# Kernel optimization log

Measured on AMD Instinct MI355X. Metric: run time of the kernel, lower is better.

Reference implementation:

```python
import jax, jax.numpy as jnp
import numpy as np

N_SEND = 49152   # 12 * 64^2 HEALPix nodes
N_REC = 65536    # 256x256 receiver grid
N_EDGES = 262144 # N_REC * 4 nearest senders
D_MODEL = 256
EDGE_IN, EDGE_OUT = 4, 64
LIN_IN, LIN_OUT = 320, 256
B = 2


def setup_inputs() -> dict:
    key = jax.random.key(0)
    ks = jax.random.split(key, 8)
    x = jax.random.normal(ks[0], (B, N_SEND, D_MODEL), dtype=jnp.float32)
    senders = jax.random.randint(ks[1], (N_EDGES,), 0, N_SEND, dtype=jnp.int32)
    receivers = jax.random.randint(ks[2], (N_EDGES,), 0, N_REC, dtype=jnp.int32)
    edge_index = jnp.stack([senders, receivers], axis=0)
    edge_attr = jax.random.normal(ks[3], (N_EDGES, EDGE_IN), dtype=jnp.float32)
    s = lambda fan_in: 1.0 / np.sqrt(fan_in)
    return {
        "x": x,
        "edge_index": edge_index,
        "edge_attr": edge_attr,
        "ee_w1": jax.random.normal(ks[4], (EDGE_IN, EDGE_OUT), dtype=jnp.float32) * s(EDGE_IN),
        "ee_b1": jnp.zeros((EDGE_OUT,), dtype=jnp.float32),
        "ee_w2": jax.random.normal(ks[5], (EDGE_OUT, EDGE_OUT), dtype=jnp.float32) * s(EDGE_OUT),
        "ee_b2": jnp.zeros((EDGE_OUT,), dtype=jnp.float32),
        "ff_w1": jax.random.normal(ks[6], (LIN_IN, LIN_OUT), dtype=jnp.float32) * s(LIN_IN),
        "ff_b1": jnp.zeros((LIN_OUT,), dtype=jnp.float32),
        "ff_w2": jax.random.normal(ks[7], (LIN_OUT, LIN_OUT), dtype=jnp.float32) * s(LIN_OUT),
        "ff_b2": jnp.zeros((LIN_OUT,), dtype=jnp.float32),
    }


def reference(x, edge_index, edge_attr,
              ee_w1, ee_b1, ee_w2, ee_b2,
              ff_w1, ff_b1, ff_w2, ff_b2):
    senders, receivers = edge_index[0], edge_index[1]
    # edge embedder MLP: [E, edge_in] -> [E, edge_out]
    h = jax.nn.relu(edge_attr @ ee_w1 + ee_b1)
    edge_feat = h @ ee_w2 + ee_b2                       # [E, edge_out]
    # gather sender node features: [B, E, d_model]
    v_s = x[:, senders, :]
    # concat with broadcast edge features: [B, E, d_model + edge_out]
    ef = jnp.broadcast_to(edge_feat[None], (x.shape[0],) + edge_feat.shape)
    v_s_prime = jnp.concatenate([v_s, ef], axis=-1)
    # scatter-sum onto receiver nodes: [B, n_rec, lin_in]
    v_m_sum = jnp.zeros((x.shape[0], N_REC, v_s_prime.shape[-1]), dtype=x.dtype)
    v_m_sum = v_m_sum.at[:, receivers, :].add(v_s_prime)
    # g2m feedforward: [B, n_rec, lin_out]
    h2 = jax.nn.relu(v_m_sum @ ff_w1 + ff_b1)
    return h2 @ ff_w2 + ff_b2
```

## Files before the change

kernel.cpp:

```cpp
#include <hip/hip_runtime.h>
#include <hip/hip_bf16.h>

#define N_SEND 49152
#define N_REC  65536
#define N_EDGES 262144
#define D_MODEL 256
#define EDGE_IN 4
#define EDGE_OUT 64
#define LIN_IN 320
#define LIN_OUT 256
#define BATCH 2

#define GBM 64

typedef __attribute__((ext_vector_type(4))) float f32x4;
typedef __attribute__((ext_vector_type(8))) short bf16x8;

static __device__ __forceinline__ unsigned short f2bf(float f) {
    union { float f; unsigned u; } v; v.f = f;
    unsigned r = v.u + 0x7FFF + ((v.u >> 16) & 1);
    return (unsigned short)(r >> 16);
}
static __device__ __forceinline__ float bf2f(unsigned short h) {
    union { unsigned u; float f; } v; v.u = ((unsigned)h) << 16; return v.f;
}

static __device__ __forceinline__ void async_copy16(void* lds_ptr, const void* g_ptr) {
    __builtin_amdgcn_global_load_lds(
        (const __attribute__((address_space(1))) void*)g_ptr,
        (__attribute__((address_space(3))) void*)lds_ptr, 16, 0, 0);
}

__global__ __launch_bounds__(256) void prep_fused(
    const float* __restrict__ x, unsigned short* __restrict__ xb, int nconv,
    const int* __restrict__ receivers, const float* __restrict__ edge_attr,
    const float* __restrict__ ee_w1, const float* __restrict__ ee_b1,
    const float* __restrict__ ee_w2, const float* __restrict__ ee_b2,
    unsigned short* __restrict__ efs, int* __restrict__ counts,
    const float* __restrict__ w1, const float* __restrict__ w2,
    unsigned short* __restrict__ w1t, unsigned short* __restrict__ w2t)
{
    __shared__ __align__(16) unsigned short h_lds[256 * EDGE_OUT];

    const int bid = blockIdx.x;
    const int tid = threadIdx.x;

    if (bid < nconv) {
        const size_t i = ((size_t)bid * 256 + tid) * 8;
        const float4 v0 = *(const float4*)&x[i];
        const float4 v1 = *(const float4*)&x[i + 4];
        bf16x8 o;
        o[0] = (short)f2bf(v0.x); o[1] = (short)f2bf(v0.y);
        o[2] = (short)f2bf(v0.z); o[3] = (short)f2bf(v0.w);
        o[4] = (short)f2bf(v1.x); o[5] = (short)f2bf(v1.y);
        o[6] = (short)f2bf(v1.z); o[7] = (short)f2bf(v1.w);
        *(bf16x8*)&xb[i] = o;
        return;
    }
    const int b2 = bid - nconv;

    if (b2 < N_EDGES / 256) {
        const int e0 = b2 * 256;
        atomicAdd(&counts[receivers[e0 + tid]], 1);

        {
            const float4 ea = *(const float4*)&edge_attr[(size_t)(e0 + tid) * EDGE_IN];
#pragma unroll
            for (int kb = 0; kb < 8; ++kb) {
                bf16x8 hv;
#pragma unroll
                for (int j = 0; j < 8; ++j) {
                    const int k = kb * 8 + j;
                    float a = ee_b1[k];
                    a += ea.x * ee_w1[0 * EDGE_OUT + k];
                    a += ea.y * ee_w1[1 * EDGE_OUT + k];
                    a += ea.z * ee_w1[2 * EDGE_OUT + k];
                    a += ea.w * ee_w1[3 * EDGE_OUT + k];
                    hv[j] = (short)f2bf(fmaxf(a, 0.0f));
                }
                *(bf16x8*)&h_lds[tid * EDGE_OUT + ((kb ^ (tid & 7)) * 8)] = hv;
            }
        }

        const int lane = tid & 63, wave = tid >> 6;
        const int n16 = lane & 15, hi = lane >> 4;

        bf16x8 bfr[2][4];
#pragma unroll
        for (int ch = 0; ch < 2; ++ch)
#pragma unroll
            for (int c = 0; c < 4; ++c) {
                bf16x8 b;
#pragma unroll
                for (int j = 0; j < 8; ++j) {
                    const int k = ch * 32 + hi * 8 + j;
                    b[j] = (short)f2bf(ee_w2[k * EDGE_OUT + 16 * c + n16]);
                }
                bfr[ch][c] = b;
            }

        f32x4 acc[4][4];
#pragma unroll
        for (int c = 0; c < 4; ++c) {
            const float bv = ee_b2[16 * c + n16];
#pragma unroll
            for (int t = 0; t < 4; ++t) {
                acc[t][c][0] = bv; acc[t][c][1] = bv; acc[t][c][2] = bv; acc[t][c][3] = bv;
            }
        }

#pragma unroll
        for (int ch = 0; ch < 2; ++ch) {
            bf16x8 af[4];
#pragma unroll
            for (int t = 0; t < 4; ++t) {
                const int row = 64 * wave + 16 * t + n16;
                const int slot = (4 * ch + hi) ^ (row & 7);
                af[t] = *(const bf16x8*)&h_lds[row * EDGE_OUT + slot * 8];
            }
#pragma unroll
            for (int c = 0; c < 4; ++c)
#pragma unroll
                for (int t = 0; t < 4; ++t)
                    acc[t][c] = __builtin_amdgcn_mfma_f32_16x16x32_bf16(af[t], bfr[ch][c], acc[t][c], 0, 0, 0);
        }

#pragma unroll
        for (int t = 0; t < 4; ++t)
#pragma unroll
            for (int c = 0; c < 4; ++c)
#pragma unroll
                for (int r = 0; r < 4; ++r)
                    efs[(size_t)(e0 + 64 * wave + 16 * t + 4 * hi + r) * EDGE_OUT + 16 * c + n16] =
                        f2bf(acc[t][c][r]);
        return;
    }

    {
        const int t3 = (b2 - N_EDGES / 256) * 256 + tid;
        if (t3 < 256 * LIN_IN) {
            const int n = t3 / LIN_IN, k = t3 - n * LIN_IN;
            w1t[t3] = f2bf(w1[k * LIN_OUT + n]);
        } else {
            const int t2 = t3 - 256 * LIN_IN;
            if (t2 < 256 * 256) {
                const int n = t2 >> 8, k = t2 & 255;
                w2t[t2] = f2bf(w2[k * LIN_OUT + n]);
            }
        }
    }
}

__global__ __launch_bounds__(1024) void scan_kernel(
    const int* __restrict__ counts, int* __restrict__ row_ptr,
    int* __restrict__ cursor)
{
    __shared__ int sums[1024];
    const int t = threadIdx.x;
    const int4* c4 = (const int4*)(counts + t * 64);

    int s = 0;
#pragma unroll
    for (int i = 0; i < 16; ++i) { const int4 c = c4[i]; s += c.x + c.y + c.z + c.w; }
    sums[t] = s;
    __syncthreads();

    for (int off = 1; off < 1024; off <<= 1) {
        const int v = (t >= off) ? sums[t - off] : 0;
        __syncthreads();
        sums[t] += v;
        __syncthreads();
    }

    int run = sums[t] - s;
#pragma unroll
    for (int i = 0; i < 16; ++i) {
        const int4 c = c4[i];
        int4 w;
        w.x = run; w.y = run + c.x; w.z = w.y + c.y; w.w = w.z + c.z;
        run = w.w + c.w;
        ((int4*)(row_ptr + t * 64))[i] = w;
        ((int4*)(cursor + t * 64))[i] = w;
    }
    if (t == 1023) row_ptr[N_REC] = run;
}

__global__ __launch_bounds__(256) void fill_kernel(
    const int* __restrict__ senders, const int* __restrict__ receivers,
    int* __restrict__ cursor, int* __restrict__ edge_order,
    int* __restrict__ ssort)
{
    const int e = blockIdx.x * 256 + threadIdx.x;
    const int r = receivers[e];
    const int pos = atomicAdd(&cursor[r], 1);
    edge_order[pos] = e;
    ssort[pos] = senders[e];
}

template<bool XB>
__global__ __launch_bounds__(256) void gather_kernel(
    const float* __restrict__ x,
    const unsigned short* __restrict__ xb,
    const unsigned short* __restrict__ efs,
    const int* __restrict__ row_ptr,
    const int* __restrict__ edge_order,
    const int* __restrict__ ssort,
    unsigned short* __restrict__ vmb)
{
    const int lane = threadIdx.x & 63;
    const int wave = threadIdx.x >> 6;
    const int r = blockIdx.x * 4 + wave;
    const int beg = row_ptr[r], end = row_ptr[r + 1];
    const int half = lane >> 5, l2 = lane & 31;

    float ax[8] = {0, 0, 0, 0, 0, 0, 0, 0};
    float ae[8] = {0, 0, 0, 0, 0, 0, 0, 0};

    for (int chunk = beg; chunk < end; chunk += 64) {
        const int n = min(64, end - chunk);
        int myidx = 0, myeidx = 0;
        if (chunk + lane < end) {
            myidx = ssort[chunk + lane];
            myeidx = edge_order[chunk + lane];
        }
        for (int i = 0; i < n; ++i) {
            const int s = __shfl(myidx, i);
            const int e = __shfl(myeidx, i);
            const size_t rowbase = (size_t)(half ? N_SEND + s : s) * D_MODEL;
            if (XB) {
                const bf16x8 v = *(const bf16x8*)&xb[rowbase + l2 * 8];
#pragma unroll
                for (int j = 0; j < 8; ++j) ax[j] += bf2f((unsigned short)v[j]);
            } else {
                const float4 v0 = *(const float4*)&x[rowbase + l2 * 8];
                const float4 v1 = *(const float4*)&x[rowbase + l2 * 8 + 4];
                ax[0] += v0.x; ax[1] += v0.y; ax[2] += v0.z; ax[3] += v0.w;
                ax[4] += v1.x; ax[5] += v1.y; ax[6] += v1.z; ax[7] += v1.w;
            }
            if (lane < 8) {
                const bf16x8 w = *(const bf16x8*)&efs[(size_t)e * EDGE_OUT + lane * 8];
#pragma unroll
                for (int j = 0; j < 8; ++j) ae[j] += bf2f((unsigned short)w[j]);
            }
        }
    }

    bf16x8 o;
#pragma unroll
    for (int j = 0; j < 8; ++j) o[j] = (short)f2bf(ax[j]);
    *(bf16x8*)&vmb[((size_t)(half * N_REC + r)) * LIN_IN + l2 * 8] = o;
    if (lane < 8) {
        bf16x8 oe;
#pragma unroll
        for (int j = 0; j < 8; ++j) oe[j] = (short)f2bf(ae[j]);
        *(bf16x8*)&vmb[((size_t)r) * LIN_IN + D_MODEL + lane * 8] = oe;
        *(bf16x8*)&vmb[((size_t)(N_REC + r)) * LIN_IN + D_MODEL + lane * 8] = oe;
    }
}

__global__ __launch_bounds__(256, 2) void node_mlp_fused(
    const unsigned short* __restrict__ vmb,
    const unsigned short* __restrict__ w1t,
    const float* __restrict__ b1,
    const unsigned short* __restrict__ w2t,
    const float* __restrict__ b2,
    float* __restrict__ out)
{
    __shared__ __align__(16) char lds[73728];

    const int tid  = threadIdx.x;
    const int lane = tid & 63, wc = tid >> 6;
    const int n16  = lane & 15, hi = lane >> 4;
    const size_t row0 = (size_t)blockIdx.x * GBM;
    char* const hbase = lds + 40960;

    const int f_l = (n16 & 3) ^ ((n16 >> 2) & 3);
    const int hsl = (hi ^ f_l) << 4;

    auto stageA = [&](int kk, int buf) {
        const int row = tid >> 2;
        const int sl = (tid & 3) ^ ((row & 3) ^ ((row >> 2) & 3));
        const unsigned short* g = vmb + (row0 + row) * LIN_IN + kk + sl * 8;
        char* l = lds + (buf << 12) + ((tid >> 6) << 10);
        async_copy16(l, g);
    };
    auto stageB = [&](const unsigned short* BT, int ldk, int kk, int buf) {
#pragma unroll
        for (int p = 0; p < 4; ++p) {
            const int i = p * 256 + tid, row = i >> 2;
            const int sl = (i & 3) ^ ((row & 3) ^ ((row >> 2) & 3));
            const unsigned short* g = BT + (size_t)row * ldk + kk + sl * 8;
            char* l = lds + 8192 + (buf << 14) + (p << 12) + ((tid >> 6) << 10);
            async_copy16(l, g);
        }
    };

    stageA(0, 0); stageB(w1t, LIN_IN, 0, 0);

    f32x4 acc[4][4];
#pragma unroll
    for (int c = 0; c < 4; ++c) {
        const float bv = b1[64 * wc + 16 * c + n16];
#pragma unroll
        for (int t = 0; t < 4; ++t) {
            acc[t][c][0] = bv; acc[t][c][1] = bv; acc[t][c][2] = bv; acc[t][c][3] = bv;
        }
    }

    int cur = 0;
    for (int step = 0; step < LIN_IN / 32; ++step) {
        __syncthreads();
        if (step + 1 < LIN_IN / 32) {
            stageA((step + 1) * 32, cur ^ 1);
            stageB(w1t, LIN_IN, (step + 1) * 32, cur ^ 1);
        }
        bf16x8 af[4], bf[4];
        const char* Ab = lds + (cur << 12);
        const char* Bb = lds + 8192 + (cur << 14);
#pragma unroll
        for (int t = 0; t < 4; ++t)
            af[t] = *(const bf16x8*)(Ab + (16 * t + n16) * 64 + hsl);
#pragma unroll
        for (int c = 0; c < 4; ++c)
            bf[c] = *(const bf16x8*)(Bb + (64 * wc + 16 * c + n16) * 64 + hsl);
#pragma unroll
        for (int c = 0; c < 4; ++c)
#pragma unroll
            for (int t = 0; t < 4; ++t)
                acc[t][c] = __builtin_amdgcn_mfma_f32_16x16x32_bf16(af[t], bf[c], acc[t][c], 0, 0, 0);
        cur ^= 1;
    }

    stageB(w2t, LIN_OUT, 0, 0);

#pragma unroll
    for (int t = 0; t < 4; ++t)
#pragma unroll
        for (int c = 0; c < 4; ++c) {
            const int col = 64 * wc + 16 * c + n16;
            const int kc = col >> 5;
            const int b  = (col & 31) * 2;
            const int gslot = b >> 4;
#pragma unroll
            for (int r = 0; r < 4; ++r) {
                const int lrow = 16 * t + 4 * hi + r;
                const int f = (lrow & 3) ^ ((lrow >> 2) & 3);
                *(unsigned short*)(hbase + (kc << 12) + lrow * 64 + (((gslot ^ f) << 4) | (b & 15))) =
                    f2bf(fmaxf(acc[t][c][r], 0.0f));
            }
        }
    __syncthreads();

    f32x4 acc2[4][4];
#pragma unroll
    for (int c = 0; c < 4; ++c) {
        const float bv = b2[64 * wc + 16 * c + n16];
#pragma unroll
        for (int t = 0; t < 4; ++t) {
            acc2[t][c][0] = bv; acc2[t][c][1] = bv; acc2[t][c][2] = bv; acc2[t][c][3] = bv;
        }
    }

    cur = 0;
    for (int step = 0; step < LIN_OUT / 32; ++step) {
        if (step + 1 < LIN_OUT / 32) stageB(w2t, LIN_OUT, (step + 1) * 32, cur ^ 1);

        bf16x8 af[4], bf[4];
        const char* Hb = hbase + (step << 12);
        const char* Bb = lds + 8192 + (cur << 14);
#pragma unroll
        for (int t = 0; t < 4; ++t)
            af[t] = *(const bf16x8*)(Hb + (16 * t + n16) * 64 + hsl);
#pragma unroll
        for (int c = 0; c < 4; ++c)
            bf[c] = *(const bf16x8*)(Bb + (64 * wc + 16 * c + n16) * 64 + hsl);
#pragma unroll
        for (int c = 0; c < 4; ++c)
#pragma unroll
            for (int t = 0; t < 4; ++t)
                acc2[t][c] = __builtin_amdgcn_mfma_f32_16x16x32_bf16(af[t], bf[c], acc2[t][c], 0, 0, 0);

        __syncthreads();
        cur ^= 1;
    }

#pragma unroll
    for (int t = 0; t < 4; ++t)
#pragma unroll
        for (int c = 0; c < 4; ++c)
#pragma unroll
            for (int r = 0; r < 4; ++r)
                out[(row0 + 16 * t + 4 * hi + r) * LIN_OUT + 64 * wc + 16 * c + n16] =
                    acc2[t][c][r];
}

extern "C" void kernel_launch(void* const* d_in, const int* in_sizes, int n_in,
                              void* d_out, int out_size, void* d_ws, size_t ws_size,
                              hipStream_t stream) {
    const float* x         = (const float*)d_in[0];
    const int*   edge_idx  = (const int*)d_in[1];
    const float* edge_attr = (const float*)d_in[2];
    const float* ee_w1     = (const float*)d_in[3];
    const float* ee_b1     = (const float*)d_in[4];
    const float* ee_w2     = (const float*)d_in[5];
    const float* ee_b2     = (const float*)d_in[6];
    const float* ff_w1     = (const float*)d_in[7];
    const float* ff_b1     = (const float*)d_in[8];
    const float* ff_w2     = (const float*)d_in[9];
    const float* ff_b2     = (const float*)d_in[10];
    float* out = (float*)d_out;

    const int* senders   = edge_idx;
    const int* receivers = edge_idx + N_EDGES;

    char* ws = (char*)d_ws;
    size_t off = 0;
    auto alloc = [&](size_t bytes) { char* p = ws + off; off += (bytes + 511) & ~511ull; return p; };

    unsigned short* vmb = (unsigned short*)alloc((size_t)BATCH * N_REC * LIN_IN * 2);
    unsigned short* efs = (unsigned short*)alloc((size_t)N_EDGES * EDGE_OUT * 2);
    unsigned short* w1t = (unsigned short*)alloc((size_t)256 * LIN_IN * 2);
    unsigned short* w2t = (unsigned short*)alloc((size_t)256 * LIN_OUT * 2);
    int* row_ptr        = (int*)alloc((size_t)(N_REC + 1) * 4);
    int* counts         = (int*)alloc((size_t)N_REC * 4);
    int* cursor         = (int*)alloc((size_t)N_REC * 4);
    int* edge_order     = (int*)alloc((size_t)N_EDGES * 4);
    int* ssort          = (int*)alloc((size_t)N_EDGES * 4);
    const size_t base_need = off;
    unsigned short* xb  = (unsigned short*)(ws + off);
    const size_t xb_bytes = (size_t)BATCH * N_SEND * D_MODEL * 2;
    const bool use_xb = (ws_size >= base_need + xb_bytes);

    hipMemsetAsync(counts, 0, (size_t)N_REC * 4, stream);

    const int nconv = use_xb ? (int)((size_t)BATCH * N_SEND * D_MODEL / 8 / 256) : 0;
    const int prep_grid = nconv + N_EDGES / 256 + (256 * LIN_IN + 256 * LIN_OUT + 255) / 256;
    prep_fused<<<prep_grid, 256, 0, stream>>>(
        x, xb, nconv, receivers, edge_attr, ee_w1, ee_b1, ee_w2, ee_b2,
        efs, counts, ff_w1, ff_w2, w1t, w2t);

    scan_kernel<<<1, 1024, 0, stream>>>(counts, row_ptr, cursor);

    fill_kernel<<<N_EDGES / 256, 256, 0, stream>>>(
        senders, receivers, cursor, edge_order, ssort);

    if (use_xb) {
        gather_kernel<true><<<N_REC / 4, 256, 0, stream>>>(
            x, xb, efs, row_ptr, edge_order, ssort, vmb);
    } else {
        gather_kernel<false><<<N_REC / 4, 256, 0, stream>>>(
            x, xb, efs, row_ptr, edge_order, ssort, vmb);
    }

    node_mlp_fused<<<(BATCH * N_REC) / GBM, 256, 0, stream>>>(
        vmb, w1t, ff_b1, w2t, ff_b2, out);
}
```

Measured before the change: 238.5 us.

## Fuse gather-scatter aggregation into node MLP kernel, keeping aggregated tile in LDS

```diff
diff --git a/kernel.cpp b/kernel.cpp
--- a/kernel.cpp
+++ b/kernel.cpp
@@ -197,69 +197,12 @@
     ssort[pos] = senders[e];
 }
 
-template<bool XB>
-__global__ __launch_bounds__(256) void gather_kernel(
-    const float* __restrict__ x,
+__global__ __launch_bounds__(256, 2) void node_fused(
     const unsigned short* __restrict__ xb,
     const unsigned short* __restrict__ efs,
     const int* __restrict__ row_ptr,
     const int* __restrict__ edge_order,
     const int* __restrict__ ssort,
-    unsigned short* __restrict__ vmb)
-{
-    const int lane = threadIdx.x & 63;
-    const int wave = threadIdx.x >> 6;
-    const int r = blockIdx.x * 4 + wave;
-    const int beg = row_ptr[r], end = row_ptr[r + 1];
-    const int half = lane >> 5, l2 = lane & 31;
-
-    float ax[8] = {0, 0, 0, 0, 0, 0, 0, 0};
-    float ae[8] = {0, 0, 0, 0, 0, 0, 0, 0};
-
-    for (int chunk = beg; chunk < end; chunk += 64) {
-        const int n = min(64, end - chunk);
-        int myidx = 0, myeidx = 0;
-        if (chunk + lane < end) {
-            myidx = ssort[chunk + lane];
-            myeidx = edge_order[chunk + lane];
-        }
-        for (int i = 0; i < n; ++i) {
-            const int s = __shfl(myidx, i);
-            const int e = __shfl(myeidx, i);
-            const size_t rowbase = (size_t)(half ? N_SEND + s : s) * D_MODEL;
-            if (XB) {
-                const bf16x8 v = *(const bf16x8*)&xb[rowbase + l2 * 8];
-#pragma unroll
-                for (int j = 0; j < 8; ++j) ax[j] += bf2f((unsigned short)v[j]);
-            } else {
-                const float4 v0 = *(const float4*)&x[rowbase + l2 * 8];
-                const float4 v1 = *(const float4*)&x[rowbase + l2 * 8 + 4];
-                ax[0] += v0.x; ax[1] += v0.y; ax[2] += v0.z; ax[3] += v0.w;
-                ax[4] += v1.x; ax[5] += v1.y; ax[6] += v1.z; ax[7] += v1.w;
-            }
-            if (lane < 8) {
-                const bf16x8 w = *(const bf16x8*)&efs[(size_t)e * EDGE_OUT + lane * 8];
-#pragma unroll
-                for (int j = 0; j < 8; ++j) ae[j] += bf2f((unsigned short)w[j]);
-            }
-        }
-    }
-
-    bf16x8 o;
-#pragma unroll
-    for (int j = 0; j < 8; ++j) o[j] = (short)f2bf(ax[j]);
-    *(bf16x8*)&vmb[((size_t)(half * N_REC + r)) * LIN_IN + l2 * 8] = o;
-    if (lane < 8) {
-        bf16x8 oe;
-#pragma unroll
-        for (int j = 0; j < 8; ++j) oe[j] = (short)f2bf(ae[j]);
-        *(bf16x8*)&vmb[((size_t)r) * LIN_IN + D_MODEL + lane * 8] = oe;
-        *(bf16x8*)&vmb[((size_t)(N_REC + r)) * LIN_IN + D_MODEL + lane * 8] = oe;
-    }
-}
-
-__global__ __launch_bounds__(256, 2) void node_mlp_fused(
-    const unsigned short* __restrict__ vmb,
     const unsigned short* __restrict__ w1t,
     const float* __restrict__ b1,
     const unsigned short* __restrict__ w2t,
@@ -269,38 +212,88 @@
     __shared__ __align__(16) char lds[73728];
 
     const int tid  = threadIdx.x;
-    const int lane = tid & 63, wc = tid >> 6;
+    const int lane = tid & 63, wv = tid >> 6;
     const int n16  = lane & 15, hi = lane >> 4;
     const size_t row0 = (size_t)blockIdx.x * GBM;
-    char* const hbase = lds + 40960;
+    const int batch = (int)(row0 >> 16);
+    const int rbase = (int)(row0 & 65535);
+    char* const vmbase = lds + 32768;
 
     const int f_l = (n16 & 3) ^ ((n16 >> 2) & 3);
     const int hsl = (hi ^ f_l) << 4;
 
-    auto stageA = [&](int kk, int buf) {
-        const int row = tid >> 2;
-        const int sl = (tid & 3) ^ ((row & 3) ^ ((row >> 2) & 3));
-        const unsigned short* g = vmb + (row0 + row) * LIN_IN + kk + sl * 8;
-        char* l = lds + (buf << 12) + ((tid >> 6) << 10);
-        async_copy16(l, g);
-    };
     auto stageB = [&](const unsigned short* BT, int ldk, int kk, int buf) {
 #pragma unroll
         for (int p = 0; p < 4; ++p) {
             const int i = p * 256 + tid, row = i >> 2;
             const int sl = (i & 3) ^ ((row & 3) ^ ((row >> 2) & 3));
             const unsigned short* g = BT + (size_t)row * ldk + kk + sl * 8;
-            char* l = lds + 8192 + (buf << 14) + (p << 12) + ((tid >> 6) << 10);
+            char* l = lds + (buf << 14) + (p << 12) + ((tid >> 6) << 10);
             async_copy16(l, g);
         }
     };
 
-    stageA(0, 0); stageB(w1t, LIN_IN, 0, 0);
+    stageB(w1t, LIN_IN, 0, 0);
+
+    {
+        const int half = lane >> 5, l2 = lane & 31;
+        const size_t xbase = (size_t)batch * N_SEND * D_MODEL;
+        for (int it = 0; it < 8; ++it) {
+            const int rloc = wv * 16 + it * 2 + half;
+            const int ra = rbase + wv * 16 + it * 2;
+            const int pa = row_ptr[ra], pb = row_ptr[ra + 1], pc = row_ptr[ra + 2];
+            const int beg = half ? pb : pa;
+            const int mydeg = half ? (pc - pb) : (pb - pa);
+            const int mx = max(pb - pa, pc - pb);
+
+            float ax[8] = {0, 0, 0, 0, 0, 0, 0, 0};
+            float ae[8] = {0, 0, 0, 0, 0, 0, 0, 0};
+            for (int c0 = 0; c0 < mx; c0 += 32) {
+                int myidx = 0, myeidx = 0;
+                if (c0 + l2 < mydeg) {
+                    myidx = ssort[beg + c0 + l2];
+                    myeidx = edge_order[beg + c0 + l2];
+                }
+                const int n = min(32, mx - c0);
+                for (int i = 0; i < n; i += 4) {
+                    bf16x8 vx[4], ve[4];
+#pragma unroll
+                    for (int u = 0; u < 4; ++u) {
+                        const int s = __shfl(myidx, half * 32 + i + u);
+                        const int e = __shfl(myeidx, half * 32 + i + u);
+                        const bool p = (c0 + i + u < mydeg);
+                        bf16x8 z = {0, 0, 0, 0, 0, 0, 0, 0};
+                        vx[u] = z; ve[u] = z;
+                        if (p) vx[u] = *(const bf16x8*)&xb[xbase + (size_t)s * D_MODEL + l2 * 8];
+                        if (p && l2 < 8) ve[u] = *(const bf16x8*)&efs[(size_t)e * EDGE_OUT + l2 * 8];
+                    }
+#pragma unroll
+                    for (int u = 0; u < 4; ++u)
+#pragma unroll
+                        for (int j = 0; j < 8; ++j) {
+                            ax[j] += bf2f((unsigned short)vx[u][j]);
+                            ae[j] += bf2f((unsigned short)ve[u][j]);
+                        }
+                }
+            }
+            const int fr = (rloc & 3) ^ ((rloc >> 2) & 3);
+            bf16x8 o;
+#pragma unroll
+            for (int j = 0; j < 8; ++j) o[j] = (short)f2bf(ax[j]);
+            *(bf16x8*)(vmbase + ((l2 >> 2) << 12) + rloc * 64 + (((l2 & 3) ^ fr) << 4)) = o;
+            if (l2 < 8) {
+                bf16x8 oe;
+#pragma unroll
+                for (int j = 0; j < 8; ++j) oe[j] = (short)f2bf(ae[j]);
+                *(bf16x8*)(vmbase + ((8 + (l2 >> 2)) << 12) + rloc * 64 + (((l2 & 3) ^ fr) << 4)) = oe;
+            }
+        }
+    }
 
     f32x4 acc[4][4];
 #pragma unroll
     for (int c = 0; c < 4; ++c) {
-        const float bv = b1[64 * wc + 16 * c + n16];
+        const float bv = b1[64 * wv + 16 * c + n16];
 #pragma unroll
         for (int t = 0; t < 4; ++t) {
             acc[t][c][0] = bv; acc[t][c][1] = bv; acc[t][c][2] = bv; acc[t][c][3] = bv;
@@ -310,19 +303,18 @@
     int cur = 0;
     for (int step = 0; step < LIN_IN / 32; ++step) {
         __syncthreads();
-        if (step + 1 < LIN_IN / 32) {
-            stageA((step + 1) * 32, cur ^ 1);
+        if (step + 1 < LIN_IN / 32)
             stageB(w1t, LIN_IN, (step + 1) * 32, cur ^ 1);
-        }
+
         bf16x8 af[4], bf[4];
-        const char* Ab = lds + (cur << 12);
-        const char* Bb = lds + 8192 + (cur << 14);
+        const char* Ab = vmbase + (step << 12);
+        const char* Bb = lds + (cur << 14);
 #pragma unroll
         for (int t = 0; t < 4; ++t)
             af[t] = *(const bf16x8*)(Ab + (16 * t + n16) * 64 + hsl);
 #pragma unroll
         for (int c = 0; c < 4; ++c)
-            bf[c] = *(const bf16x8*)(Bb + (64 * wc + 16 * c + n16) * 64 + hsl);
+            bf[c] = *(const bf16x8*)(Bb + (64 * wv + 16 * c + n16) * 64 + hsl);
 #pragma unroll
         for (int c = 0; c < 4; ++c)
 #pragma unroll
@@ -337,7 +329,7 @@
     for (int t = 0; t < 4; ++t)
 #pragma unroll
         for (int c = 0; c < 4; ++c) {
-            const int col = 64 * wc + 16 * c + n16;
+            const int col = 64 * wv + 16 * c + n16;
             const int kc = col >> 5;
             const int b  = (col & 31) * 2;
             const int gslot = b >> 4;
@@ -345,7 +337,7 @@
             for (int r = 0; r < 4; ++r) {
                 const int lrow = 16 * t + 4 * hi + r;
                 const int f = (lrow & 3) ^ ((lrow >> 2) & 3);
-                *(unsigned short*)(hbase + (kc << 12) + lrow * 64 + (((gslot ^ f) << 4) | (b & 15))) =
+                *(unsigned short*)(vmbase + (kc << 12) + lrow * 64 + (((gslot ^ f) << 4) | (b & 15))) =
                     f2bf(fmaxf(acc[t][c][r], 0.0f));
             }
         }
@@ -354,7 +346,7 @@
     f32x4 acc2[4][4];
 #pragma unroll
     for (int c = 0; c < 4; ++c) {
-        const float bv = b2[64 * wc + 16 * c + n16];
+        const float bv = b2[64 * wv + 16 * c + n16];
 #pragma unroll
         for (int t = 0; t < 4; ++t) {
             acc2[t][c][0] = bv; acc2[t][c][1] = bv; acc2[t][c][2] = bv; acc2[t][c][3] = bv;
@@ -366,14 +358,14 @@
         if (step + 1 < LIN_OUT / 32) stageB(w2t, LIN_OUT, (step + 1) * 32, cur ^ 1);
 
         bf16x8 af[4], bf[4];
-        const char* Hb = hbase + (step << 12);
-        const char* Bb = lds + 8192 + (cur << 14);
+        const char* Hb = vmbase + (step << 12);
+        const char* Bb = lds + (cur << 14);
 #pragma unroll
         for (int t = 0; t < 4; ++t)
             af[t] = *(const bf16x8*)(Hb + (16 * t + n16) * 64 + hsl);
 #pragma unroll
         for (int c = 0; c < 4; ++c)
-            bf[c] = *(const bf16x8*)(Bb + (64 * wc + 16 * c + n16) * 64 + hsl);
+            bf[c] = *(const bf16x8*)(Bb + (64 * wv + 16 * c + n16) * 64 + hsl);
 #pragma unroll
         for (int c = 0; c < 4; ++c)
 #pragma unroll
@@ -390,7 +382,7 @@
         for (int c = 0; c < 4; ++c)
 #pragma unroll
             for (int r = 0; r < 4; ++r)
-                out[(row0 + 16 * t + 4 * hi + r) * LIN_OUT + 64 * wc + 16 * c + n16] =
+                out[(row0 + 16 * t + 4 * hi + r) * LIN_OUT + 64 * wv + 16 * c + n16] =
                     acc2[t][c][r];
 }
 
@@ -417,8 +409,8 @@
     size_t off = 0;
     auto alloc = [&](size_t bytes) { char* p = ws + off; off += (bytes + 511) & ~511ull; return p; };
 
-    unsigned short* vmb = (unsigned short*)alloc((size_t)BATCH * N_REC * LIN_IN * 2);
     unsigned short* efs = (unsigned short*)alloc((size_t)N_EDGES * EDGE_OUT * 2);
+    unsigned short* xb  = (unsigned short*)alloc((size_t)BATCH * N_SEND * D_MODEL * 2);
     unsigned short* w1t = (unsigned short*)alloc((size_t)256 * LIN_IN * 2);
     unsigned short* w2t = (unsigned short*)alloc((size_t)256 * LIN_OUT * 2);
     int* row_ptr        = (int*)alloc((size_t)(N_REC + 1) * 4);
@@ -426,14 +418,10 @@
     int* cursor         = (int*)alloc((size_t)N_REC * 4);
     int* edge_order     = (int*)alloc((size_t)N_EDGES * 4);
     int* ssort          = (int*)alloc((size_t)N_EDGES * 4);
-    const size_t base_need = off;
-    unsigned short* xb  = (unsigned short*)(ws + off);
-    const size_t xb_bytes = (size_t)BATCH * N_SEND * D_MODEL * 2;
-    const bool use_xb = (ws_size >= base_need + xb_bytes);
 
     hipMemsetAsync(counts, 0, (size_t)N_REC * 4, stream);
 
-    const int nconv = use_xb ? (int)((size_t)BATCH * N_SEND * D_MODEL / 8 / 256) : 0;
+    const int nconv = (int)((size_t)BATCH * N_SEND * D_MODEL / 8 / 256);
     const int prep_grid = nconv + N_EDGES / 256 + (256 * LIN_IN + 256 * LIN_OUT + 255) / 256;
     prep_fused<<<prep_grid, 256, 0, stream>>>(
         x, xb, nconv, receivers, edge_attr, ee_w1, ee_b1, ee_w2, ee_b2,
@@ -444,14 +432,6 @@
     fill_kernel<<<N_EDGES / 256, 256, 0, stream>>>(
         senders, receivers, cursor, edge_order, ssort);
 
-    if (use_xb) {
-        gather_kernel<true><<<N_REC / 4, 256, 0, stream>>>(
-            x, xb, efs, row_ptr, edge_order, ssort, vmb);
-    } else {
-        gather_kernel<false><<<N_REC / 4, 256, 0, stream>>>(
-            x, xb, efs, row_ptr, edge_order, ssort, vmb);
-    }
-
-    node_mlp_fused<<<(BATCH * N_REC) / GBM, 256, 0, stream>>>(
-        vmb, w1t, ff_b1, w2t, ff_b2, out);
-}
+    node_fused<<<(BATCH * N_REC) / GBM, 256, 0, stream>>>(
+        xb, efs, row_ptr, edge_order, ssort, w1t, ff_b1, w2t, ff_b2, out);
+}
```

Result: slower. 265.8 us (+11.5%).
